# Kernel tuning notes

Hardware: AMD Instinct MI355X
Metric: run time of the kernel (lower is better)

## Reference

```python
import jax, jax.numpy as jnp
import numpy as np

# Module config (matches init_kwargs)
IC, OC, K, R, C, STRIDE = 128, 256, 3, 64, 64, 1
TAPS = 576
B = 16
BIAS_LEN = 128
H_OUT = (R - K) // STRIDE + 1  # 62
W_OUT = (C - K) // STRIDE + 1  # 62


def setup_inputs() -> dict:
    key = jax.random.key(0)
    k1, k2, k3 = jax.random.split(key, 3)
    rng = np.random.default_rng(0)
    # Per output channel, choose TAPS distinct (c, ky, kx) taps out of IC*K*K.
    all_taps = IC * K * K
    tap_ids = np.stack([rng.choice(all_taps, TAPS, replace=False) for _ in range(OC)])  # [OC, TAPS]
    c = tap_ids // (K * K)
    rem = tap_ids % (K * K)
    ky, kx = rem // K, rem % K
    # Flattened gather index into a [IC, R, C] image, exactly as the CUDA module builds it.
    image_weight_index = (c * (R * C) + ky * C + kx).astype(np.int32).reshape(-1)  # [OC*TAPS]
    filter_lengths = np.full(OC, TAPS, dtype=np.int32)
    start_points = (np.arange(OC, dtype=np.int64) * TAPS).astype(np.int32)
    bias_index = rng.choice(OC, BIAS_LEN, replace=False).astype(np.int32)
    return {
        "images": jax.random.normal(k1, (B, IC, R, C), jnp.float32),
        "weight_value": jax.random.normal(k2, (OC * TAPS,), jnp.float32) * 0.05,
        "image_weight_index": jnp.asarray(image_weight_index),
        "filter_lengths": jnp.asarray(filter_lengths),
        "start_points": jnp.asarray(start_points),
        "bias_index": jnp.asarray(bias_index),
        "bias_value": jax.random.normal(k3, (BIAS_LEN,), jnp.float32),
    }


def reference(images, weight_value, image_weight_index, filter_lengths, start_points, bias_index, bias_value):
    nnz = weight_value.shape[0]
    # Taps are stored contiguously per output channel (start_points = cumsum of filter_lengths).
    oc_ids = jnp.repeat(jnp.arange(OC), filter_lengths, total_repeat_length=nnz)
    # Decode flattened image index back to (in_channel, ky, kx).
    c = image_weight_index // (R * C)
    rem = image_weight_index % (R * C)
    ky, kx = rem // C, rem % C
    # Scatter sparse taps into a dense OIHW kernel; the gather-conv math is then
    # an exact VALID strided cross-correlation.
    W = jnp.zeros((OC, IC, K, K), images.dtype).at[oc_ids, c, ky, kx].add(weight_value)
    out = jax.lax.conv_general_dilated(
        images, W, window_strides=(STRIDE, STRIDE), padding="VALID",
        dimension_numbers=("NCHW", "OIHW", "NCHW"))  # [B, OC, H_OUT, W_OUT]
    # Conditional bias: channel oc gets bias_value[j] for each j with bias_index[j] == oc.
    bias = jnp.zeros((OC,), images.dtype).at[bias_index].add(bias_value)
    return out + bias[None, :, None, None]
```

## Files before the change

### kernel.cpp

```cpp
#include <hip/hip_runtime.h>
#include <stdint.h>

#define IC 128
#define OC 256
#define RR 64
#define CCOLS 64
#define HO 62
#define WO 62
#define NB 16

#define W9T_BYTES (9 * OC * IC * 2)
#define CHUNK_STRIDE 8192
#define LDS_TOTAL 49216

typedef __bf16 bf16x8 __attribute__((ext_vector_type(8)));
typedef float f32x16 __attribute__((ext_vector_type(16)));

__device__ __forceinline__ unsigned short f2bf(float f) {
    unsigned u = __builtin_bit_cast(unsigned, f);
    u += 0x7FFFu + ((u >> 16) & 1u);
    return (unsigned short)(u >> 16);
}

__global__ void prep_weights(const float* __restrict__ wv,
                             const int* __restrict__ iwi,
                             const int* __restrict__ flen,
                             const int* __restrict__ sp,
                             unsigned char* __restrict__ W9Tf,
                             const int* __restrict__ bias_index,
                             const float* __restrict__ bias_value,
                             float* __restrict__ bias_dense, int nbias) {
    if (blockIdx.x == OC) {
        int t = threadIdx.x;
        if (t < OC) bias_dense[t] = 0.f;
        __syncthreads();
        if (t < nbias) atomicAdd(&bias_dense[bias_index[t]], bias_value[t]);
        return;
    }
    const int oc = blockIdx.x;
    const int s = sp[oc];
    const int n = flen[oc];
    const int g = oc >> 5;
    for (int t = threadIdx.x; t < n; t += blockDim.x) {
        const int ix = iwi[s + t];
        const int c = ix >> 12;
        const int rem = ix & 4095;
        const int ky = rem >> 6, kx = rem & 63;
        const int kp = ky * 3 + kx;
        const int ck = c >> 4;
        const int khalf = (c >> 3) & 1;
        const int lane = (oc & 31) + (khalf << 5);
        const size_t off = (size_t)(kp * 8 + ck) * CHUNK_STRIDE +
                           g * 1024 + lane * 16 + (c & 7) * 2;
        *(unsigned short*)(W9Tf + off) = f2bf(wv[s + t]);
    }
}

#define KSTEP1(IDX, AV0, AV1, VN, LGN)                                        \
  {                                                                           \
    if constexpr ((IDX) + 1 < 72) {                                           \
      constexpr int i1_ = (IDX) + 1;                                          \
      constexpr int kp1_ = i1_ >> 3, ck1_ = i1_ & 7;                          \
      constexpr int o1_ = (kp1_ / 3) * 16384 + ck1_ * 2048 + (kp1_ % 3) * 16; \
      asm volatile("ds_read_b128 %0, %1" : "=v"(b0n) : "v"(bB + o1_));        \
      asm volatile("ds_read_b128 %0, %1" : "=v"(b1n) : "v"(bB + o1_ + 512));  \
    }                                                                         \
    asm volatile("s_waitcnt vmcnt(" VN ") lgkmcnt(" LGN ")"                   \
                 : "+v"(AV0), "+v"(AV1));                                     \
    __builtin_amdgcn_sched_barrier(0);                                        \
    c00 = __builtin_amdgcn_mfma_f32_32x32x16_bf16(AV0, b0c, c00, 0, 0, 0);    \
    c10 = __builtin_amdgcn_mfma_f32_32x32x16_bf16(AV1, b0c, c10, 0, 0, 0);    \
    c01 = __builtin_amdgcn_mfma_f32_32x32x16_bf16(AV0, b1c, c01, 0, 0, 0);    \
    c11 = __builtin_amdgcn_mfma_f32_32x32x16_bf16(AV1, b1c, c11, 0, 0, 0);    \
    if constexpr ((IDX) + 4 < 72) {                                           \
      asm volatile("global_load_dwordx4 %0, %1, off"                          \
                   : "=v"(AV0)                                                \
                   : "v"(pA0 + (size_t)((IDX) + 4) * CHUNK_STRIDE));          \
      asm volatile("global_load_dwordx4 %0, %1, off"                          \
                   : "=v"(AV1)                                                \
                   : "v"(pA1 + (size_t)((IDX) + 4) * CHUNK_STRIDE));          \
    }                                                                         \
    if constexpr ((IDX) + 1 < 72) { b0c = b0n; b1c = b1n; }                   \
  }

#define K4(I) KSTEP1((I)+0, a0S0, a1S0, "6", "2") \
              KSTEP1((I)+1, a0S1, a1S1, "6", "2") \
              KSTEP1((I)+2, a0S2, a1S2, "6", "2") \
              KSTEP1((I)+3, a0S3, a1S3, "6", "2")

__global__ __launch_bounds__(256, 3) void conv_mfma(
    const float* __restrict__ images,
    const unsigned char* __restrict__ W9Tf,
    const float* __restrict__ bias_dense,
    float* __restrict__ out)
{
    const int y = blockIdx.x;
    const int b = blockIdx.y;
    const int t = threadIdx.x;
    const int w = t >> 6;
    const int l = t & 63;
    const int lm = l & 31;
    const int lhi = l >> 5;

    __shared__ unsigned char lds[LDS_TOTAL];

    const float* __restrict__ imgb = images + (size_t)b * (IC * RR * CCOLS);

    {
        const int xs = t & 63;
        const int og = t >> 6;
        #pragma unroll
        for (int krow = 0; krow < 3; ++krow) {
            #pragma unroll
            for (int h = 0; h < 4; ++h) {
                const int o = og + 4 * h;
                const int c0 = o * 8;
                const float* __restrict__ p =
                    imgb + (size_t)c0 * (RR * CCOLS) + (y + krow) * CCOLS + xs;
                unsigned v0, v1, v2, v3;
                v0 = (unsigned)f2bf(p[0])              | ((unsigned)f2bf(p[RR * CCOLS])     << 16);
                v1 = (unsigned)f2bf(p[2 * RR * CCOLS]) | ((unsigned)f2bf(p[3 * RR * CCOLS]) << 16);
                v2 = (unsigned)f2bf(p[4 * RR * CCOLS]) | ((unsigned)f2bf(p[5 * RR * CCOLS]) << 16);
                v3 = (unsigned)f2bf(p[6 * RR * CCOLS]) | ((unsigned)f2bf(p[7 * RR * CCOLS]) << 16);
                *(uint4*)(lds + krow * 16384 + o * 1024 + xs * 16) =
                    make_uint4(v0, v1, v2, v3);
            }
        }
    }

    const unsigned char* __restrict__ pA0 = W9Tf + (2 * w + 0) * 1024 + l * 16;
    const unsigned char* __restrict__ pA1 = W9Tf + (2 * w + 1) * 1024 + l * 16;
    const unsigned bB = (unsigned)(uintptr_t)(lds + lhi * 1024 + lm * 16);

    __syncthreads();

    bf16x8 a0S0, a0S1, a0S2, a0S3, a1S0, a1S1, a1S2, a1S3;
    bf16x8 b0c, b1c, b0n, b1n;
    asm volatile("global_load_dwordx4 %0, %1, off" : "=v"(a0S0) : "v"(pA0));
    asm volatile("global_load_dwordx4 %0, %1, off" : "=v"(a1S0) : "v"(pA1));
    asm volatile("global_load_dwordx4 %0, %1, off" : "=v"(a0S1) : "v"(pA0 + CHUNK_STRIDE));
    asm volatile("global_load_dwordx4 %0, %1, off" : "=v"(a1S1) : "v"(pA1 + CHUNK_STRIDE));
    asm volatile("global_load_dwordx4 %0, %1, off" : "=v"(a0S2) : "v"(pA0 + 2 * CHUNK_STRIDE));
    asm volatile("global_load_dwordx4 %0, %1, off" : "=v"(a1S2) : "v"(pA1 + 2 * CHUNK_STRIDE));
    asm volatile("global_load_dwordx4 %0, %1, off" : "=v"(a0S3) : "v"(pA0 + 3 * CHUNK_STRIDE));
    asm volatile("global_load_dwordx4 %0, %1, off" : "=v"(a1S3) : "v"(pA1 + 3 * CHUNK_STRIDE));
    asm volatile("ds_read_b128 %0, %1" : "=v"(b0c) : "v"(bB));
    asm volatile("ds_read_b128 %0, %1" : "=v"(b1c) : "v"(bB + 512u));

    f32x16 c00 = {}, c01 = {}, c10 = {}, c11 = {};

    K4(0) K4(4) K4(8) K4(12) K4(16) K4(20) K4(24) K4(28) K4(32)
    K4(36) K4(40) K4(44) K4(48) K4(52) K4(56) K4(60) K4(64)
    KSTEP1(68, a0S0, a1S0, "6", "2") KSTEP1(69, a0S1, a1S1, "4", "2")
    KSTEP1(70, a0S2, a1S2, "2", "2") KSTEP1(71, a0S3, a1S3, "0", "0")

    #pragma unroll
    for (int m = 0; m < 2; ++m) {
        const int ocw = (2 * w + m) * 32;
        const f32x16 d0 = m ? c10 : c00;
        const f32x16 d1 = m ? c11 : c01;
        #pragma unroll
        for (int r = 0; r < 16; ++r) {
            const int oc = ocw + (r & 3) + 8 * (r >> 2) + 4 * lhi;
            const float bv = bias_dense[oc];
            const size_t ob = (((size_t)b * OC + oc) * HO + y) * WO;
            out[ob + lm] = d0[r] + bv;
            if (lm < 30)
                out[ob + 32 + lm] = d1[r] + bv;
        }
    }
}

extern "C" void kernel_launch(void* const* d_in, const int* in_sizes, int n_in,
                              void* d_out, int out_size, void* d_ws, size_t ws_size,
                              hipStream_t stream) {
    const float* images             = (const float*)d_in[0];
    const float* weight_value       = (const float*)d_in[1];
    const int*   image_weight_index = (const int*)d_in[2];
    const int*   filter_lengths     = (const int*)d_in[3];
    const int*   start_points       = (const int*)d_in[4];
    const int*   bias_index         = (const int*)d_in[5];
    const float* bias_value         = (const float*)d_in[6];
    float* out = (float*)d_out;

    unsigned char* W9Tf = (unsigned char*)d_ws;
    float* bias_dense = (float*)((char*)d_ws + W9T_BYTES);

    hipMemsetAsync(d_ws, 0, W9T_BYTES, stream);
    prep_weights<<<OC + 1, 256, 0, stream>>>(weight_value, image_weight_index,
                                             filter_lengths, start_points, W9Tf,
                                             bias_index, bias_value, bias_dense,
                                             in_sizes[5]);

    dim3 grid(HO, NB);
    conv_mfma<<<grid, 256, 0, stream>>>(images, W9Tf, bias_dense, out);
}
```

Before: 65.38 us.

## Compute two output rows per block to reuse weight loads across rows

Each block now computes two adjacent output rows, staging four input rows in LDS and issuing eight MFMAs per weight fragment, so every global weight load is shared by twice the work. The grid halves to 31x16 blocks, accumulator registers double, and launch bounds drop to one block per SM. MFMA sections are also wrapped in s_setprio. The risks are lower occupancy from the larger LDS and register footprint, and fewer blocks than before to fill the GPU.

```diff
diff --git a/kernel.cpp b/kernel.cpp
--- a/kernel.cpp
+++ b/kernel.cpp
@@ -11,7 +11,7 @@
 
 #define W9T_BYTES (9 * OC * IC * 2)
 #define CHUNK_STRIDE 8192
-#define LDS_TOTAL 49216
+#define LDS_TOTAL 65600
 
 typedef __bf16 bf16x8 __attribute__((ext_vector_type(8)));
 typedef float f32x16 __attribute__((ext_vector_type(16)));
@@ -61,17 +61,26 @@
     if constexpr ((IDX) + 1 < 72) {                                           \
       constexpr int i1_ = (IDX) + 1;                                          \
       constexpr int kp1_ = i1_ >> 3, ck1_ = i1_ & 7;                          \
-      constexpr int o1_ = (kp1_ / 3) * 16384 + ck1_ * 2048 + (kp1_ % 3) * 16; \
-      asm volatile("ds_read_b128 %0, %1" : "=v"(b0n) : "v"(bB + o1_));        \
-      asm volatile("ds_read_b128 %0, %1" : "=v"(b1n) : "v"(bB + o1_ + 512));  \
+      constexpr int ky1_ = kp1_ / 3;                                          \
+      constexpr int o1_ = ky1_ * 16384 + ck1_ * 2048 + (kp1_ % 3) * 16;       \
+      asm volatile("ds_read_b128 %0, %1" : "=v"(b00n) : "v"(bB + o1_));       \
+      asm volatile("ds_read_b128 %0, %1" : "=v"(b01n) : "v"(bB + o1_ + 512)); \
+      asm volatile("ds_read_b128 %0, %1" : "=v"(b10n) : "v"(bB + o1_ + 16384)); \
+      asm volatile("ds_read_b128 %0, %1" : "=v"(b11n) : "v"(bB + o1_ + 16384 + 512)); \
     }                                                                         \
     asm volatile("s_waitcnt vmcnt(" VN ") lgkmcnt(" LGN ")"                   \
                  : "+v"(AV0), "+v"(AV1));                                     \
     __builtin_amdgcn_sched_barrier(0);                                        \
-    c00 = __builtin_amdgcn_mfma_f32_32x32x16_bf16(AV0, b0c, c00, 0, 0, 0);    \
-    c10 = __builtin_amdgcn_mfma_f32_32x32x16_bf16(AV1, b0c, c10, 0, 0, 0);    \
-    c01 = __builtin_amdgcn_mfma_f32_32x32x16_bf16(AV0, b1c, c01, 0, 0, 0);    \
-    c11 = __builtin_amdgcn_mfma_f32_32x32x16_bf16(AV1, b1c, c11, 0, 0, 0);    \
+    __builtin_amdgcn_s_setprio(1);                                            \
+    c000 = __builtin_amdgcn_mfma_f32_32x32x16_bf16(AV0, b00c, c000, 0, 0, 0); \
+    c100 = __builtin_amdgcn_mfma_f32_32x32x16_bf16(AV1, b00c, c100, 0, 0, 0); \
+    c001 = __builtin_amdgcn_mfma_f32_32x32x16_bf16(AV0, b01c, c001, 0, 0, 0); \
+    c101 = __builtin_amdgcn_mfma_f32_32x32x16_bf16(AV1, b01c, c101, 0, 0, 0); \
+    c010 = __builtin_amdgcn_mfma_f32_32x32x16_bf16(AV0, b10c, c010, 0, 0, 0); \
+    c110 = __builtin_amdgcn_mfma_f32_32x32x16_bf16(AV1, b10c, c110, 0, 0, 0); \
+    c011 = __builtin_amdgcn_mfma_f32_32x32x16_bf16(AV0, b11c, c011, 0, 0, 0); \
+    c111 = __builtin_amdgcn_mfma_f32_32x32x16_bf16(AV1, b11c, c111, 0, 0, 0); \
+    __builtin_amdgcn_s_setprio(0);                                            \
     if constexpr ((IDX) + 4 < 72) {                                           \
       asm volatile("global_load_dwordx4 %0, %1, off"                          \
                    : "=v"(AV0)                                                \
@@ -80,21 +89,23 @@
                    : "=v"(AV1)                                                \
                    : "v"(pA1 + (size_t)((IDX) + 4) * CHUNK_STRIDE));          \
     }                                                                         \
-    if constexpr ((IDX) + 1 < 72) { b0c = b0n; b1c = b1n; }                   \
+    if constexpr ((IDX) + 1 < 72) {                                           \
+      b00c = b00n; b01c = b01n; b10c = b10n; b11c = b11n;                     \
+    }                                                                         \
   }
 
-#define K4(I) KSTEP1((I)+0, a0S0, a1S0, "6", "2") \
-              KSTEP1((I)+1, a0S1, a1S1, "6", "2") \
-              KSTEP1((I)+2, a0S2, a1S2, "6", "2") \
-              KSTEP1((I)+3, a0S3, a1S3, "6", "2")
-
-__global__ __launch_bounds__(256, 3) void conv_mfma(
+#define K4(I) KSTEP1((I)+0, a0S0, a1S0, "6", "4") \
+              KSTEP1((I)+1, a0S1, a1S1, "6", "4") \
+              KSTEP1((I)+2, a0S2, a1S2, "6", "4") \
+              KSTEP1((I)+3, a0S3, a1S3, "6", "4")
+
+__global__ __launch_bounds__(256, 1) void conv_mfma(
     const float* __restrict__ images,
     const unsigned char* __restrict__ W9Tf,
     const float* __restrict__ bias_dense,
     float* __restrict__ out)
 {
-    const int y = blockIdx.x;
+    const int y0 = blockIdx.x * 2;
     const int b = blockIdx.y;
     const int t = threadIdx.x;
     const int w = t >> 6;
@@ -110,13 +121,13 @@
         const int xs = t & 63;
         const int og = t >> 6;
         #pragma unroll
-        for (int krow = 0; krow < 3; ++krow) {
+        for (int krow = 0; krow < 4; ++krow) {
             #pragma unroll
             for (int h = 0; h < 4; ++h) {
                 const int o = og + 4 * h;
                 const int c0 = o * 8;
                 const float* __restrict__ p =
-                    imgb + (size_t)c0 * (RR * CCOLS) + (y + krow) * CCOLS + xs;
+                    imgb + (size_t)c0 * (RR * CCOLS) + (y0 + krow) * CCOLS + xs;
                 unsigned v0, v1, v2, v3;
                 v0 = (unsigned)f2bf(p[0])              | ((unsigned)f2bf(p[RR * CCOLS])     << 16);
                 v1 = (unsigned)f2bf(p[2 * RR * CCOLS]) | ((unsigned)f2bf(p[3 * RR * CCOLS]) << 16);
@@ -135,7 +146,7 @@
     __syncthreads();
 
     bf16x8 a0S0, a0S1, a0S2, a0S3, a1S0, a1S1, a1S2, a1S3;
-    bf16x8 b0c, b1c, b0n, b1n;
+    bf16x8 b00c, b01c, b10c, b11c, b00n, b01n, b10n, b11n;
     asm volatile("global_load_dwordx4 %0, %1, off" : "=v"(a0S0) : "v"(pA0));
     asm volatile("global_load_dwordx4 %0, %1, off" : "=v"(a1S0) : "v"(pA1));
     asm volatile("global_load_dwordx4 %0, %1, off" : "=v"(a0S1) : "v"(pA0 + CHUNK_STRIDE));
@@ -144,29 +155,38 @@
     asm volatile("global_load_dwordx4 %0, %1, off" : "=v"(a1S2) : "v"(pA1 + 2 * CHUNK_STRIDE));
     asm volatile("global_load_dwordx4 %0, %1, off" : "=v"(a0S3) : "v"(pA0 + 3 * CHUNK_STRIDE));
     asm volatile("global_load_dwordx4 %0, %1, off" : "=v"(a1S3) : "v"(pA1 + 3 * CHUNK_STRIDE));
-    asm volatile("ds_read_b128 %0, %1" : "=v"(b0c) : "v"(bB));
-    asm volatile("ds_read_b128 %0, %1" : "=v"(b1c) : "v"(bB + 512u));
-
-    f32x16 c00 = {}, c01 = {}, c10 = {}, c11 = {};
+    asm volatile("ds_read_b128 %0, %1" : "=v"(b00c) : "v"(bB));
+    asm volatile("ds_read_b128 %0, %1" : "=v"(b01c) : "v"(bB + 512u));
+    asm volatile("ds_read_b128 %0, %1" : "=v"(b10c) : "v"(bB + 16384u));
+    asm volatile("ds_read_b128 %0, %1" : "=v"(b11c) : "v"(bB + 16384u + 512u));
+
+    f32x16 c000 = {}, c001 = {}, c010 = {}, c011 = {};
+    f32x16 c100 = {}, c101 = {}, c110 = {}, c111 = {};
 
     K4(0) K4(4) K4(8) K4(12) K4(16) K4(20) K4(24) K4(28) K4(32)
     K4(36) K4(40) K4(44) K4(48) K4(52) K4(56) K4(60) K4(64)
-    KSTEP1(68, a0S0, a1S0, "6", "2") KSTEP1(69, a0S1, a1S1, "4", "2")
-    KSTEP1(70, a0S2, a1S2, "2", "2") KSTEP1(71, a0S3, a1S3, "0", "0")
+    KSTEP1(68, a0S0, a1S0, "6", "4") KSTEP1(69, a0S1, a1S1, "4", "4")
+    KSTEP1(70, a0S2, a1S2, "2", "4") KSTEP1(71, a0S3, a1S3, "0", "0")
 
     #pragma unroll
     for (int m = 0; m < 2; ++m) {
         const int ocw = (2 * w + m) * 32;
-        const f32x16 d0 = m ? c10 : c00;
-        const f32x16 d1 = m ? c11 : c01;
+        const f32x16 d00 = m ? c100 : c000;
+        const f32x16 d01 = m ? c101 : c001;
+        const f32x16 d10 = m ? c110 : c010;
+        const f32x16 d11 = m ? c111 : c011;
         #pragma unroll
         for (int r = 0; r < 16; ++r) {
             const int oc = ocw + (r & 3) + 8 * (r >> 2) + 4 * lhi;
             const float bv = bias_dense[oc];
-            const size_t ob = (((size_t)b * OC + oc) * HO + y) * WO;
-            out[ob + lm] = d0[r] + bv;
+            const size_t ob0 = (((size_t)b * OC + oc) * HO + y0) * WO;
+            out[ob0 + lm] = d00[r] + bv;
             if (lm < 30)
-                out[ob + 32 + lm] = d1[r] + bv;
+                out[ob0 + 32 + lm] = d01[r] + bv;
+            const size_t ob1 = ob0 + WO;
+            out[ob1 + lm] = d10[r] + bv;
+            if (lm < 30)
+                out[ob1 + 32 + lm] = d11[r] + bv;
         }
     }
 }
@@ -192,6 +212,6 @@
                                              bias_index, bias_value, bias_dense,
                                              in_sizes[5]);
 
-    dim3 grid(HO, NB);
+    dim3 grid(HO / 2, NB);
     conv_mfma<<<grid, 256, 0, stream>>>(images, W9Tf, bias_dense, out);
 }
```

Result: faster. 60.06 us (-8.1%).
